# Optimization experiments

Measured on AMD Instinct MI355X. Metric: run time of the kernel, lower is better.

Reference implementation:

```python
import jax, jax.numpy as jnp
import numpy as np

B, LQ, E = 32, 64, 512
NF, FL, D = 10, 40, 512
H, A, R, V = 512, 512, 1024, 50257
NEG = -1e9


def setup_inputs() -> dict:
    key = jax.random.key(0)
    ks = jax.random.split(key, 20)
    s = 0.02
    return {
        'bq': jax.random.normal(ks[0], (B, LQ, E), jnp.float32),
        'fe': jax.random.normal(ks[1], (B, NF, FL, D), jnp.float32),
        'h0': jax.random.normal(ks[2], (B, H), jnp.float32),
        'c0': jax.random.normal(ks[3], (B, H), jnp.float32),
        'prev_emb': jax.random.normal(ks[4], (B, E), jnp.float32),
        'Wq_enc': jax.random.normal(ks[5], (E, A), jnp.float32) * s,
        'Wq_dec': jax.random.normal(ks[6], (H, A), jnp.float32) * s,
        'vq': jax.random.normal(ks[7], (A,), jnp.float32) * s,
        'Wf_enc': jax.random.normal(ks[8], (D, A), jnp.float32) * s,
        'Wf_dec': jax.random.normal(ks[9], (H, A), jnp.float32) * s,
        'vf': jax.random.normal(ks[10], (A,), jnp.float32) * s,
        'lstm_kernel': jax.random.normal(ks[11], (E + D + E, 4 * H), jnp.float32) * s,
        'lstm_rec': jax.random.normal(ks[12], (H, 4 * H), jnp.float32) * s,
        'lstm_bias': jnp.zeros((4 * H,), jnp.float32),
        'Wr': jax.random.normal(ks[13], (H, R), jnp.float32) * s,
        'br': jnp.zeros((R,), jnp.float32),
        'Ur': jax.random.normal(ks[14], (E + D + E, R), jnp.float32) * s,
        'bu': jnp.zeros((R,), jnp.float32),
        'Vr': jax.random.normal(ks[15], (E, R), jnp.float32) * s,
        'bv': jnp.zeros((R,), jnp.float32),
        'Wy': jax.random.normal(ks[16], (R // 2, V), jnp.float32) * s,
        'by': jnp.zeros((V,), jnp.float32),
        'q_mask': jnp.ones((B, LQ), bool),
        'f_mask': jnp.ones((B, NF, FL), bool),
    }


def reference(bq, fe, h0, c0, prev_emb, Wq_enc, Wq_dec, vq, Wf_enc, Wf_dec, vf,
              lstm_kernel, lstm_rec, lstm_bias, Wr, br, Ur, bu, Vr, bv, Wy, by,
              q_mask, f_mask):
    # --- question additive attention: softmax over seq axis ---
    q_scores = jnp.tanh(jnp.einsum('ble,ea->bla', bq, Wq_enc)
                        + (h0 @ Wq_dec)[:, None, :]) @ vq          # [B, Lq]
    q_logits = jnp.where(q_mask, q_scores, NEG)
    q_w = jax.nn.softmax(q_logits, axis=1)
    q_vec = jnp.einsum('bl,ble->be', q_w, bq)                      # [B, E]

    # --- facts attention: score all positions, keep top fact_len, renormalize ---
    f_scores = jnp.tanh(jnp.einsum('bnld,da->bnla', fe, Wf_enc)
                        + (h0 @ Wf_dec)[:, None, None, :]) @ vf    # [B, nf, fl]
    f_logits = jnp.where(f_mask, f_scores, NEG).reshape(fe.shape[0], -1)  # [B, nf*fl]
    fe_flat = fe.reshape(fe.shape[0], -1, fe.shape[-1])            # [B, nf*fl, D]
    top_scores, top_idx = jax.lax.top_k(f_logits, fe.shape[2])     # k = fact_len
    top_w = jax.nn.softmax(top_scores, axis=-1)                    # [B, fl]
    sel = jnp.take_along_axis(fe_flat, top_idx[:, :, None], axis=1)  # [B, fl, D]
    f_vec = jnp.einsum('bk,bkd->bd', top_w, sel)                   # [B, D]

    # --- LSTM cell (keras gate order i, f, g, o) ---
    x = jnp.concatenate([prev_emb, f_vec, q_vec], axis=1)          # [B, 2E+D]
    z = x @ lstm_kernel + h0 @ lstm_rec + lstm_bias
    i, f, g, o = jnp.split(z, 4, axis=-1)
    c = jax.nn.sigmoid(f) * c0 + jax.nn.sigmoid(i) * jnp.tanh(g)
    h = jax.nn.sigmoid(o) * jnp.tanh(c)

    # --- readout: three-branch dense + maxout + vocab projection ---
    r = (h @ Wr + br) + (x @ Ur + bu) + (q_vec @ Vr + bv)          # [B, R]
    m = r.reshape(r.shape[0], R // 2, 2).max(axis=-1)              # maxout -> [B, R/2]
    logits = m @ Wy + by                                           # [B, V]
    return logits, h, c, q_vec, q_logits
```

## Files before the change

kernel.cpp:

```cpp
#include <hip/hip_runtime.h>
#include <hip/hip_bf16.h>

#define B_ 32
#define LQ_ 64
#define E_ 512
#define NFL_ 400
#define D_ 512
#define H_ 512
#define A_ 512
#define R_ 1024
#define V_ 50257
#define X_ 1536
#define FL_ 40

#define O_H  1608224L
#define O_C  1624608L
#define O_QV 1640992L
#define O_QL 1657376L

typedef __bf16 bf16;
typedef __bf16 bf16x2 __attribute__((ext_vector_type(2)));
typedef __bf16 bf16x8 __attribute__((ext_vector_type(8)));
typedef float f32x4 __attribute__((ext_vector_type(4)));

__device__ inline float fexp(float x) { return __expf(x); }
__device__ inline float ftanh(float x) { return 1.0f - 2.0f / (fexp(2.0f * x) + 1.0f); }
__device__ inline float fsigm(float x) { return 1.0f / (1.0f + fexp(-x)); }

__global__ void k_transpose(const float* __restrict__ W0, const float* __restrict__ W1,
                            bf16* __restrict__ T0, bf16* __restrict__ T1) {
    __shared__ float tile[32][33];
    const float* src = blockIdx.z ? W1 : W0;
    bf16* dst = blockIdx.z ? T1 : T0;
    int k0 = blockIdx.y * 32, n0 = blockIdx.x * 32;
    int tx = threadIdx.x, ty = threadIdx.y;
    tile[ty][tx] = src[(k0 + ty) * 512 + n0 + tx];
    __syncthreads();
    dst[(n0 + ty) * 512 + k0 + tx] = (bf16)tile[tx][ty];
}

__global__ void k_proj(const float* __restrict__ h0, const float* __restrict__ Wq_dec,
                       const float* __restrict__ Wf_dec, float* __restrict__ dq,
                       float* __restrict__ df) {
    int b = blockIdx.y;
    int n = blockIdx.x * 256 + threadIdx.x;
    __shared__ float hl[H_];
    hl[threadIdx.x] = h0[b * H_ + threadIdx.x];
    hl[threadIdx.x + 256] = h0[b * H_ + threadIdx.x + 256];
    __syncthreads();
    const float* W = (n < A_) ? Wq_dec : Wf_dec;
    int col = n & 511;
    float acc = 0.f;
    #pragma unroll 8
    for (int k = 0; k < H_; ++k) acc += hl[k] * W[k * A_ + col];
    float* o = (n < A_) ? dq : df;
    o[b * A_ + col] = acc;
}

__global__ void k_copyprev(const float* __restrict__ pe, float* __restrict__ xb) {
    int idx = blockIdx.x * 256 + threadIdx.x;
    int b = idx >> 9, e = idx & 511;
    xb[b * X_ + e] = pe[idx];
}

__launch_bounds__(256)
__global__ void k_attn(const float* __restrict__ Amat, const bf16* __restrict__ Bt,
                       const float* __restrict__ proj, const float* __restrict__ vvec,
                       float* __restrict__ outv, int rows_per_b) {
    __shared__ bf16 al[32][520];
    int tid = threadIdx.x;
    int row0 = blockIdx.x * 32;
    #pragma unroll 8
    for (int it = 0; it < 32; ++it) {
        int i2 = it * 256 + tid;
        int r = i2 >> 8, c2 = i2 & 255;
        float2 f = *(const float2*)(Amat + (long)(row0 + r) * 512 + c2 * 2);
        bf16x2 t; t[0] = (bf16)f.x; t[1] = (bf16)f.y;
        *(bf16x2*)&al[r][c2 * 2] = t;
    }
    __syncthreads();
    int wid = tid >> 6, lane = tid & 63, q = lane >> 4, ln = lane & 15;
    int nbase = wid * 128;
    f32x4 acc[2][8];
    #pragma unroll
    for (int i = 0; i < 2; ++i)
        #pragma unroll
        for (int f = 0; f < 8; ++f) acc[i][f] = (f32x4){0.f, 0.f, 0.f, 0.f};
    for (int kk = 0; kk < 16; ++kk) {
        bf16x8 a0 = *(const bf16x8*)&al[ln][kk * 32 + q * 8];
        bf16x8 a1 = *(const bf16x8*)&al[16 + ln][kk * 32 + q * 8];
        #pragma unroll
        for (int f = 0; f < 8; ++f) {
            bf16x8 bb = *(const bf16x8*)(Bt + (long)(nbase + f * 16 + ln) * 512 + kk * 32 + q * 8);
            acc[0][f] = __builtin_amdgcn_mfma_f32_16x16x32_bf16(a0, bb, acc[0][f], 0, 0, 0);
            acc[1][f] = __builtin_amdgcn_mfma_f32_16x16x32_bf16(a1, bb, acc[1][f], 0, 0, 0);
        }
    }
    #pragma unroll
    for (int h2 = 0; h2 < 2; ++h2) {
        #pragma unroll
        for (int r = 0; r < 4; ++r) {
            int row = row0 + h2 * 16 + q * 4 + r;
            const float* pv = proj + (row / rows_per_b) * A_;
            float s = 0.f;
            #pragma unroll
            for (int f = 0; f < 8; ++f) {
                int n = nbase + f * 16 + ln;
                s += ftanh(acc[h2][f][r] + pv[n]) * vvec[n];
            }
            s += __shfl_xor(s, 1, 64); s += __shfl_xor(s, 2, 64);
            s += __shfl_xor(s, 4, 64); s += __shfl_xor(s, 8, 64);
            if (ln == 0) atomicAdd(outv + row, s);
        }
    }
}

__global__ void k_qsoft(const float* __restrict__ qsc, const float* __restrict__ bq,
                        float* __restrict__ out, float* __restrict__ xb) {
    int b = blockIdx.x, tid = threadIdx.x;
    __shared__ float w[LQ_];
    if (tid < 64) {
        float s = qsc[b * 64 + tid];
        out[O_QL + b * 64 + tid] = s;
        float m = s;
        for (int o = 32; o >= 1; o >>= 1) m = fmaxf(m, __shfl_xor(m, o, 64));
        float e = fexp(s - m);
        float sum = e;
        for (int o = 32; o >= 1; o >>= 1) sum += __shfl_xor(sum, o, 64);
        w[tid] = e / sum;
    }
    __syncthreads();
    #pragma unroll
    for (int e0 = 0; e0 < 2; ++e0) {
        int e = e0 * 256 + tid;
        float acc = 0.f;
        for (int l = 0; l < 64; ++l) acc += w[l] * bq[(b * 64 + l) * E_ + e];
        out[O_QV + b * E_ + e] = acc;
        xb[b * X_ + 1024 + e] = acc;
    }
}

__global__ void k_ftopk(const float* __restrict__ fl, const float* __restrict__ fe,
                        float* __restrict__ xb) {
    int b = blockIdx.x, tid = threadIdx.x;
    __shared__ float selw[FL_];
    __shared__ int   seli[FL_];
    if (tid < 64) {
        int lane = tid;
        float mv[7];
        #pragma unroll
        for (int s = 0; s < 7; ++s) {
            int idx = lane + s * 64;
            mv[s] = (idx < NFL_) ? fl[b * NFL_ + idx] : -1e30f;
        }
        float myv = -1e30f; int myi = 0; float v0 = 0.f;
        for (int j = 0; j < FL_; ++j) {
            float bv = -1e30f; int bi = 1 << 30;
            #pragma unroll
            for (int s = 0; s < 7; ++s) {
                int idx = lane + s * 64;
                if (mv[s] > bv || (mv[s] == bv && idx < bi)) { bv = mv[s]; bi = idx; }
            }
            for (int o = 1; o < 64; o <<= 1) {
                float ov = __shfl_xor(bv, o, 64); int oi = __shfl_xor(bi, o, 64);
                if (ov > bv || (ov == bv && oi < bi)) { bv = ov; bi = oi; }
            }
            if ((bi & 63) == lane) mv[bi >> 6] = -1e30f;
            if (lane == j) { myv = bv; myi = bi; }
            if (j == 0) v0 = bv;
        }
        float e = (lane < FL_) ? fexp(myv - v0) : 0.f;
        float sum = e;
        for (int o = 32; o >= 1; o >>= 1) sum += __shfl_xor(sum, o, 64);
        if (lane < FL_) { selw[lane] = e / sum; seli[lane] = myi; }
    }
    __syncthreads();
    #pragma unroll
    for (int d0 = 0; d0 < 2; ++d0) {
        int d = d0 * 256 + tid;
        float acc = 0.f;
        for (int j = 0; j < FL_; ++j) acc += selw[j] * fe[(long)(b * NFL_ + seli[j]) * D_ + d];
        xb[b * X_ + 512 + d] = acc;
    }
}

__launch_bounds__(256)
__global__ void k_gemm32(const float* __restrict__ Am, int lda,
                         const float* __restrict__ Bm, int N,
                         int kchunk, float* __restrict__ Cacc) {
    extern __shared__ bf16 alds[];
    int S = kchunk + 8;
    int tid = threadIdx.x;
    int k0 = blockIdx.y * kchunk;
    for (int i2 = tid; i2 < 16 * kchunk; i2 += 256) {
        int e2 = i2 * 2;
        int m = e2 / kchunk;
        int k = e2 - m * kchunk;
        float2 f = *(const float2*)(Am + (long)m * lda + k0 + k);
        bf16x2 t; t[0] = (bf16)f.x; t[1] = (bf16)f.y;
        *(bf16x2*)&alds[m * S + k] = t;
    }
    __syncthreads();
    int wid = tid >> 6, lane = tid & 63, q = lane >> 4, ln = lane & 15;
    int n = blockIdx.x * 64 + wid * 16 + ln;
    f32x4 acc0 = {0.f, 0.f, 0.f, 0.f}, acc1 = {0.f, 0.f, 0.f, 0.f};
    int steps = kchunk >> 5;
    for (int kk = 0; kk < steps; ++kk) {
        bf16x8 a0 = *(const bf16x8*)&alds[ln * S + kk * 32 + q * 8];
        bf16x8 a1 = *(const bf16x8*)&alds[(16 + ln) * S + kk * 32 + q * 8];
        bf16x8 bb;
        int kg = k0 + kk * 32 + q * 8;
        #pragma unroll
        for (int j = 0; j < 8; ++j) bb[j] = (bf16)Bm[(long)(kg + j) * N + n];
        acc0 = __builtin_amdgcn_mfma_f32_16x16x32_bf16(a0, bb, acc0, 0, 0, 0);
        acc1 = __builtin_amdgcn_mfma_f32_16x16x32_bf16(a1, bb, acc1, 0, 0, 0);
    }
    #pragma unroll
    for (int r = 0; r < 4; ++r) {
        atomicAdd(Cacc + (q * 4 + r) * N + n, acc0[r]);
        atomicAdd(Cacc + (16 + q * 4 + r) * N + n, acc1[r]);
    }
}

__global__ void k_gates(const float* __restrict__ z, const float* __restrict__ lb,
                        const float* __restrict__ c0, float* __restrict__ out,
                        float* __restrict__ hb) {
    int idx = blockIdx.x * 256 + threadIdx.x;
    int b = idx >> 9, hh = idx & 511;
    const float* zb = z + b * 2048;
    float iv = zb[hh]        + lb[hh];
    float fv = zb[512 + hh]  + lb[512 + hh];
    float gv = zb[1024 + hh] + lb[1024 + hh];
    float ov = zb[1536 + hh] + lb[1536 + hh];
    float c = fsigm(fv) * c0[idx] + fsigm(iv) * ftanh(gv);
    float h = fsigm(ov) * ftanh(c);
    out[O_H + idx] = h;
    out[O_C + idx] = c;
    hb[idx] = h;
}

__global__ void k_maxout(const float* __restrict__ r, const float* __restrict__ br,
                         const float* __restrict__ bu, const float* __restrict__ bv,
                         bf16* __restrict__ mb) {
    int idx = blockIdx.x * 256 + threadIdx.x;
    int b = idx >> 9, j = idx & 511;
    int n0 = 2 * j, n1 = 2 * j + 1;
    float r0 = r[b * R_ + n0] + br[n0] + bu[n0] + bv[n0];
    float r1 = r[b * R_ + n1] + br[n1] + bu[n1] + bv[n1];
    mb[idx] = (bf16)fmaxf(r0, r1);
}

__launch_bounds__(256)
__global__ void k_vocab(const bf16* __restrict__ mtab, const float* __restrict__ Wy,
                        const float* __restrict__ by, float* __restrict__ out) {
    __shared__ bf16 al[32][520];
    int tid = threadIdx.x;
    #pragma unroll
    for (int it = 0; it < 8; ++it) {
        int e = it * 2048 + tid * 8;
        int b = e >> 9, k = e & 511;
        *(bf16x8*)&al[b][k] = *(const bf16x8*)(mtab + e);
    }
    __syncthreads();
    int wid = tid >> 6, lane = tid & 63, q = lane >> 4, ln = lane & 15;
    int c = blockIdx.x * 64 + wid * 16 + ln;
    int cc = (c < V_) ? c : (V_ - 1);
    const float* wp = Wy + cc;
    f32x4 acc0 = {0.f, 0.f, 0.f, 0.f}, acc1 = {0.f, 0.f, 0.f, 0.f};
    float bnf[8];
    #pragma unroll
    for (int j = 0; j < 8; ++j) bnf[j] = wp[(long)(q * 8 + j) * V_];
    #pragma unroll 1
    for (int kk = 0; kk < 16; ++kk) {
        float bcur[8];
        #pragma unroll
        for (int j = 0; j < 8; ++j) bcur[j] = bnf[j];
        if (kk < 15) {
            #pragma unroll
            for (int j = 0; j < 8; ++j)
                bnf[j] = wp[(long)((kk + 1) * 32 + q * 8 + j) * V_];
        }
        bf16x8 bb;
        #pragma unroll
        for (int j = 0; j < 8; ++j) bb[j] = (bf16)bcur[j];
        bf16x8 a0 = *(const bf16x8*)&al[ln][kk * 32 + q * 8];
        bf16x8 a1 = *(const bf16x8*)&al[16 + ln][kk * 32 + q * 8];
        acc0 = __builtin_amdgcn_mfma_f32_16x16x32_bf16(a0, bb, acc0, 0, 0, 0);
        acc1 = __builtin_amdgcn_mfma_f32_16x16x32_bf16(a1, bb, acc1, 0, 0, 0);
    }
    if (c < V_) {
        float bias = by[c];
        #pragma unroll
        for (int r = 0; r < 4; ++r) {
            out[(long)(q * 4 + r) * V_ + c]      = acc0[r] + bias;
            out[(long)(16 + q * 4 + r) * V_ + c] = acc1[r] + bias;
        }
    }
}

extern "C" void kernel_launch(void* const* d_in, const int* in_sizes, int n_in,
                              void* d_out, int out_size, void* d_ws, size_t ws_size,
                              hipStream_t stream) {
    const float* bq     = (const float*)d_in[0];
    const float* fe     = (const float*)d_in[1];
    const float* h0     = (const float*)d_in[2];
    const float* c0     = (const float*)d_in[3];
    const float* prev   = (const float*)d_in[4];
    const float* Wq_enc = (const float*)d_in[5];
    const float* Wq_dec = (const float*)d_in[6];
    const float* vq     = (const float*)d_in[7];
    const float* Wf_enc = (const float*)d_in[8];
    const float* Wf_dec = (const float*)d_in[9];
    const float* vf     = (const float*)d_in[10];
    const float* lk     = (const float*)d_in[11];
    const float* lr     = (const float*)d_in[12];
    const float* lb     = (const float*)d_in[13];
    const float* Wr     = (const float*)d_in[14];
    const float* br     = (const float*)d_in[15];
    const float* Ur     = (const float*)d_in[16];
    const float* bu     = (const float*)d_in[17];
    const float* Vr     = (const float*)d_in[18];
    const float* bv     = (const float*)d_in[19];
    const float* Wy     = (const float*)d_in[20];
    const float* by     = (const float*)d_in[21];

    char* sc = (char*)d_out;
    bf16*  Wq_t = (bf16*)(sc + 0);
    bf16*  Wf_t = (bf16*)(sc + 524288);
    float* dq   = (float*)(sc + 1048576);
    float* df   = (float*)(sc + 1114112);
    float* zrec = (float*)(sc + 1179648);
    float* qsc  = (float*)(sc + 1441792);
    float* flog = (float*)(sc + 1449984);
    float* rws  = (float*)(sc + 1501184);
    float* xb   = (float*)(sc + 1632256);
    float* hb   = (float*)(sc + 1828864);
    bf16*  mb   = (bf16*)d_ws;

    float* out = (float*)d_out;

    hipMemsetAsync(zrec, 0, 452608, stream);

    k_transpose<<<dim3(16, 16, 2), dim3(32, 32), 0, stream>>>(Wq_enc, Wf_enc, Wq_t, Wf_t);
    k_proj<<<dim3(4, 32), 256, 0, stream>>>(h0, Wq_dec, Wf_dec, dq, df);
    k_copyprev<<<64, 256, 0, stream>>>(prev, xb);
    k_attn<<<64, 256, 0, stream>>>(bq, Wq_t, dq, vq, qsc, LQ_);
    k_attn<<<400, 256, 0, stream>>>(fe, Wf_t, df, vf, flog, NFL_);
    k_qsoft<<<32, 256, 0, stream>>>(qsc, bq, out, xb);
    k_ftopk<<<32, 256, 0, stream>>>(flog, fe, xb);
    k_gemm32<<<dim3(32, 4), 256, 32 * (384 + 8) * 2, stream>>>(xb, X_, lk, 2048, 384, zrec);
    k_gemm32<<<dim3(32, 2), 256, 32 * (256 + 8) * 2, stream>>>(h0, 512, lr, 2048, 256, zrec);
    k_gates<<<64, 256, 0, stream>>>(zrec, lb, c0, out, hb);
    k_gemm32<<<dim3(16, 2), 256, 32 * (256 + 8) * 2, stream>>>(hb, 512, Wr, 1024, 256, rws);
    k_gemm32<<<dim3(16, 4), 256, 32 * (384 + 8) * 2, stream>>>(xb, X_, Ur, 1024, 384, rws);
    k_gemm32<<<dim3(16, 2), 256, 32 * (256 + 8) * 2, stream>>>(xb + 1024, X_, Vr, 1024, 256, rws);
    k_maxout<<<64, 256, 0, stream>>>(rws, br, bu, bv, mb);
    k_vocab<<<786, 256, 0, stream>>>(mb, Wy, by, out);
}
```

Measured before the change: 471.7 us.

## Merge independent kernel launches into combined multi-role kernels

Merges transpose, decoder projection and prev-embedding copy into one launch. It also merges the two attention launches, the question-softmax and fact top-k kernels, and four independent GEMMs (LSTM input/recurrent plus the Ur/Vr readout branches) into single grids dispatched by block index. The aim is to cut launch overhead and the serialization between small, independent kernels. The Ur/Vr GEMMs now run before the gates kernel, and some blocks in the merged GEMM grid exit early, leaving idle blocks.

Measured after the change: 388.6 us. 1.21x faster.

```diff
diff --git a/kernel.cpp b/kernel.cpp
--- a/kernel.cpp
+++ b/kernel.cpp
@@ -27,49 +27,71 @@
 __device__ inline float ftanh(float x) { return 1.0f - 2.0f / (fexp(2.0f * x) + 1.0f); }
 __device__ inline float fsigm(float x) { return 1.0f / (1.0f + fexp(-x)); }
 
-__global__ void k_transpose(const float* __restrict__ W0, const float* __restrict__ W1,
-                            bf16* __restrict__ T0, bf16* __restrict__ T1) {
-    __shared__ float tile[32][33];
-    const float* src = blockIdx.z ? W1 : W0;
-    bf16* dst = blockIdx.z ? T1 : T0;
-    int k0 = blockIdx.y * 32, n0 = blockIdx.x * 32;
-    int tx = threadIdx.x, ty = threadIdx.y;
-    tile[ty][tx] = src[(k0 + ty) * 512 + n0 + tx];
-    __syncthreads();
-    dst[(n0 + ty) * 512 + k0 + tx] = (bf16)tile[tx][ty];
-}
-
-__global__ void k_proj(const float* __restrict__ h0, const float* __restrict__ Wq_dec,
-                       const float* __restrict__ Wf_dec, float* __restrict__ dq,
-                       float* __restrict__ df) {
-    int b = blockIdx.y;
-    int n = blockIdx.x * 256 + threadIdx.x;
-    __shared__ float hl[H_];
-    hl[threadIdx.x] = h0[b * H_ + threadIdx.x];
-    hl[threadIdx.x + 256] = h0[b * H_ + threadIdx.x + 256];
-    __syncthreads();
-    const float* W = (n < A_) ? Wq_dec : Wf_dec;
-    int col = n & 511;
-    float acc = 0.f;
-    #pragma unroll 8
-    for (int k = 0; k < H_; ++k) acc += hl[k] * W[k * A_ + col];
-    float* o = (n < A_) ? dq : df;
-    o[b * A_ + col] = acc;
-}
-
-__global__ void k_copyprev(const float* __restrict__ pe, float* __restrict__ xb) {
-    int idx = blockIdx.x * 256 + threadIdx.x;
-    int b = idx >> 9, e = idx & 511;
-    xb[b * X_ + e] = pe[idx];
-}
-
-__launch_bounds__(256)
-__global__ void k_attn(const float* __restrict__ Amat, const bf16* __restrict__ Bt,
-                       const float* __restrict__ proj, const float* __restrict__ vvec,
-                       float* __restrict__ outv, int rows_per_b) {
+__launch_bounds__(256)
+__global__ void k_pre(const float* __restrict__ W0, const float* __restrict__ W1,
+                      bf16* __restrict__ T0, bf16* __restrict__ T1,
+                      const float* __restrict__ h0, const float* __restrict__ Wq_dec,
+                      const float* __restrict__ Wf_dec, float* __restrict__ dq,
+                      float* __restrict__ df, const float* __restrict__ pe,
+                      float* __restrict__ xb) {
+    int bx = blockIdx.x;
+    if (bx < 512) {
+        __shared__ float tile[32][33];
+        int mat = bx >> 8, rest = bx & 255;
+        const float* src = mat ? W1 : W0;
+        bf16* dst = mat ? T1 : T0;
+        int k0 = (rest >> 4) * 32, n0 = (rest & 15) * 32;
+        int tx = threadIdx.x & 31, ty0 = threadIdx.x >> 5;
+        #pragma unroll
+        for (int r = 0; r < 4; ++r) {
+            int ty = ty0 + 8 * r;
+            tile[ty][tx] = src[(k0 + ty) * 512 + n0 + tx];
+        }
+        __syncthreads();
+        #pragma unroll
+        for (int r = 0; r < 4; ++r) {
+            int ty = ty0 + 8 * r;
+            dst[(n0 + ty) * 512 + k0 + tx] = (bf16)tile[tx][ty];
+        }
+    } else if (bx < 640) {
+        __shared__ float hl[H_];
+        int pb = bx - 512;
+        int b = pb >> 2;
+        int n = (pb & 3) * 256 + threadIdx.x;
+        hl[threadIdx.x] = h0[b * H_ + threadIdx.x];
+        hl[threadIdx.x + 256] = h0[b * H_ + threadIdx.x + 256];
+        __syncthreads();
+        const float* W = (n < A_) ? Wq_dec : Wf_dec;
+        int col = n & 511;
+        float acc = 0.f;
+        #pragma unroll 8
+        for (int k = 0; k < H_; ++k) acc += hl[k] * W[k * A_ + col];
+        ((n < A_) ? dq : df)[b * A_ + col] = acc;
+    } else {
+        int idx = (bx - 640) * 256 + threadIdx.x;
+        int b = idx >> 9, e = idx & 511;
+        xb[b * X_ + e] = pe[idx];
+    }
+}
+
+__launch_bounds__(256)
+__global__ void k_attn2(const float* __restrict__ bq, const float* __restrict__ fe,
+                        const bf16* __restrict__ Btq, const bf16* __restrict__ Btf,
+                        const float* __restrict__ dq, const float* __restrict__ df,
+                        const float* __restrict__ vq, const float* __restrict__ vf,
+                        float* __restrict__ qsc, float* __restrict__ flog) {
+    bool isq = blockIdx.x < 64;
+    const float* Amat = isq ? bq : fe;
+    const bf16* Bt = isq ? Btq : Btf;
+    const float* proj = isq ? dq : df;
+    const float* vvec = isq ? vq : vf;
+    float* outv = isq ? qsc : flog;
+    int rows_per_b = isq ? LQ_ : NFL_;
+    int bx = isq ? blockIdx.x : blockIdx.x - 64;
+
     __shared__ bf16 al[32][520];
     int tid = threadIdx.x;
-    int row0 = blockIdx.x * 32;
+    int row0 = bx * 32;
     #pragma unroll 8
     for (int it = 0; it < 32; ++it) {
         int i2 = it * 256 + tid;
@@ -115,83 +137,83 @@
     }
 }
 
-__global__ void k_qsoft(const float* __restrict__ qsc, const float* __restrict__ bq,
-                        float* __restrict__ out, float* __restrict__ xb) {
-    int b = blockIdx.x, tid = threadIdx.x;
-    __shared__ float w[LQ_];
-    if (tid < 64) {
-        float s = qsc[b * 64 + tid];
-        out[O_QL + b * 64 + tid] = s;
-        float m = s;
-        for (int o = 32; o >= 1; o >>= 1) m = fmaxf(m, __shfl_xor(m, o, 64));
-        float e = fexp(s - m);
-        float sum = e;
-        for (int o = 32; o >= 1; o >>= 1) sum += __shfl_xor(sum, o, 64);
-        w[tid] = e / sum;
-    }
-    __syncthreads();
-    #pragma unroll
-    for (int e0 = 0; e0 < 2; ++e0) {
-        int e = e0 * 256 + tid;
-        float acc = 0.f;
-        for (int l = 0; l < 64; ++l) acc += w[l] * bq[(b * 64 + l) * E_ + e];
-        out[O_QV + b * E_ + e] = acc;
-        xb[b * X_ + 1024 + e] = acc;
-    }
-}
-
-__global__ void k_ftopk(const float* __restrict__ fl, const float* __restrict__ fe,
-                        float* __restrict__ xb) {
-    int b = blockIdx.x, tid = threadIdx.x;
-    __shared__ float selw[FL_];
-    __shared__ int   seli[FL_];
-    if (tid < 64) {
-        int lane = tid;
-        float mv[7];
-        #pragma unroll
-        for (int s = 0; s < 7; ++s) {
-            int idx = lane + s * 64;
-            mv[s] = (idx < NFL_) ? fl[b * NFL_ + idx] : -1e30f;
-        }
-        float myv = -1e30f; int myi = 0; float v0 = 0.f;
-        for (int j = 0; j < FL_; ++j) {
-            float bv = -1e30f; int bi = 1 << 30;
+__launch_bounds__(256)
+__global__ void k_soft(const float* __restrict__ qsc, const float* __restrict__ bq,
+                       float* __restrict__ out, float* __restrict__ xb,
+                       const float* __restrict__ fl, const float* __restrict__ fe) {
+    int tid = threadIdx.x;
+    if (blockIdx.x < 32) {
+        int b = blockIdx.x;
+        __shared__ float w[LQ_];
+        if (tid < 64) {
+            float s = qsc[b * 64 + tid];
+            out[O_QL + b * 64 + tid] = s;
+            float m = s;
+            for (int o = 32; o >= 1; o >>= 1) m = fmaxf(m, __shfl_xor(m, o, 64));
+            float e = fexp(s - m);
+            float sum = e;
+            for (int o = 32; o >= 1; o >>= 1) sum += __shfl_xor(sum, o, 64);
+            w[tid] = e / sum;
+        }
+        __syncthreads();
+        #pragma unroll
+        for (int e0 = 0; e0 < 2; ++e0) {
+            int e = e0 * 256 + tid;
+            float acc = 0.f;
+            for (int l = 0; l < 64; ++l) acc += w[l] * bq[(b * 64 + l) * E_ + e];
+            out[O_QV + b * E_ + e] = acc;
+            xb[b * X_ + 1024 + e] = acc;
+        }
+    } else {
+        int b = blockIdx.x - 32;
+        __shared__ float selw[FL_];
+        __shared__ int   seli[FL_];
+        if (tid < 64) {
+            int lane = tid;
+            float mv[7];
             #pragma unroll
             for (int s = 0; s < 7; ++s) {
                 int idx = lane + s * 64;
-                if (mv[s] > bv || (mv[s] == bv && idx < bi)) { bv = mv[s]; bi = idx; }
+                mv[s] = (idx < NFL_) ? fl[b * NFL_ + idx] : -1e30f;
             }
-            for (int o = 1; o < 64; o <<= 1) {
-                float ov = __shfl_xor(bv, o, 64); int oi = __shfl_xor(bi, o, 64);
-                if (ov > bv || (ov == bv && oi < bi)) { bv = ov; bi = oi; }
+            float myv = -1e30f; int myi = 0; float v0 = 0.f;
+            for (int j = 0; j < FL_; ++j) {
+                float bv = -1e30f; int bi = 1 << 30;
+                #pragma unroll
+                for (int s = 0; s < 7; ++s) {
+                    int idx = lane + s * 64;
+                    if (mv[s] > bv || (mv[s] == bv && idx < bi)) { bv = mv[s]; bi = idx; }
+                }
+                for (int o = 1; o < 64; o <<= 1) {
+                    float ov = __shfl_xor(bv, o, 64); int oi = __shfl_xor(bi, o, 64);
+                    if (ov > bv || (ov == bv && oi < bi)) { bv = ov; bi = oi; }
+                }
+                if ((bi & 63) == lane) mv[bi >> 6] = -1e30f;
+                if (lane == j) { myv = bv; myi = bi; }
+                if (j == 0) v0 = bv;
             }
-            if ((bi & 63) == lane) mv[bi >> 6] = -1e30f;
-            if (lane == j) { myv = bv; myi = bi; }
-            if (j == 0) v0 = bv;
-        }
-        float e = (lane < FL_) ? fexp(myv - v0) : 0.f;
-        float sum = e;
-        for (int o = 32; o >= 1; o >>= 1) sum += __shfl_xor(sum, o, 64);
-        if (lane < FL_) { selw[lane] = e / sum; seli[lane] = myi; }
-    }
-    __syncthreads();
-    #pragma unroll
-    for (int d0 = 0; d0 < 2; ++d0) {
-        int d = d0 * 256 + tid;
-        float acc = 0.f;
-        for (int j = 0; j < FL_; ++j) acc += selw[j] * fe[(long)(b * NFL_ + seli[j]) * D_ + d];
-        xb[b * X_ + 512 + d] = acc;
-    }
-}
-
-__launch_bounds__(256)
-__global__ void k_gemm32(const float* __restrict__ Am, int lda,
-                         const float* __restrict__ Bm, int N,
-                         int kchunk, float* __restrict__ Cacc) {
-    extern __shared__ bf16 alds[];
+            float e = (lane < FL_) ? fexp(myv - v0) : 0.f;
+            float sum = e;
+            for (int o = 32; o >= 1; o >>= 1) sum += __shfl_xor(sum, o, 64);
+            if (lane < FL_) { selw[lane] = e / sum; seli[lane] = myi; }
+        }
+        __syncthreads();
+        #pragma unroll
+        for (int d0 = 0; d0 < 2; ++d0) {
+            int d = d0 * 256 + tid;
+            float acc = 0.f;
+            for (int j = 0; j < FL_; ++j) acc += selw[j] * fe[(long)(b * NFL_ + seli[j]) * D_ + d];
+            xb[b * X_ + 512 + d] = acc;
+        }
+    }
+}
+
+__device__ __forceinline__ void gemm32_body(
+        bf16* alds, const float* __restrict__ Am, int lda,
+        const float* __restrict__ Bm, int N, int kchunk, int k0,
+        float* __restrict__ Cacc, int gx) {
     int S = kchunk + 8;
     int tid = threadIdx.x;
-    int k0 = blockIdx.y * kchunk;
     for (int i2 = tid; i2 < 16 * kchunk; i2 += 256) {
         int e2 = i2 * 2;
         int m = e2 / kchunk;
@@ -202,7 +224,7 @@
     }
     __syncthreads();
     int wid = tid >> 6, lane = tid & 63, q = lane >> 4, ln = lane & 15;
-    int n = blockIdx.x * 64 + wid * 16 + ln;
+    int n = gx * 64 + wid * 16 + ln;
     f32x4 acc0 = {0.f, 0.f, 0.f, 0.f}, acc1 = {0.f, 0.f, 0.f, 0.f};
     int steps = kchunk >> 5;
     for (int kk = 0; kk < steps; ++kk) {
@@ -220,6 +242,31 @@
         atomicAdd(Cacc + (q * 4 + r) * N + n, acc0[r]);
         atomicAdd(Cacc + (16 + q * 4 + r) * N + n, acc1[r]);
     }
+}
+
+__launch_bounds__(256)
+__global__ void k_gemmA(const float* __restrict__ xb, const float* __restrict__ h0,
+                        const float* __restrict__ lk, const float* __restrict__ lr,
+                        const float* __restrict__ Ur, const float* __restrict__ Vr,
+                        float* __restrict__ zrec, float* __restrict__ rws) {
+    __shared__ bf16 alds[32 * 392];
+    int y = blockIdx.y;
+    const float* Am; const float* Bm; float* Cacc;
+    int lda, kchunk, k0, N;
+    if (y < 4)       { Am = xb;        lda = X_;  kchunk = 384; k0 = y * 384;        Bm = lk; N = 2048; Cacc = zrec; }
+    else if (y < 6)  { Am = h0;        lda = 512; kchunk = 256; k0 = (y - 4) * 256;  Bm = lr; N = 2048; Cacc = zrec; }
+    else if (y < 10) { Am = xb;        lda = X_;  kchunk = 384; k0 = (y - 6) * 384;  Bm = Ur; N = 1024; Cacc = rws; }
+    else             { Am = xb + 1024; lda = X_;  kchunk = 256; k0 = (y - 10) * 256; Bm = Vr; N = 1024; Cacc = rws; }
+    if ((int)blockIdx.x * 64 >= N) return;
+    gemm32_body(alds, Am, lda, Bm, N, kchunk, k0, Cacc, blockIdx.x);
+}
+
+__launch_bounds__(256)
+__global__ void k_gemm32(const float* __restrict__ Am, int lda,
+                         const float* __restrict__ Bm, int N,
+                         int kchunk, float* __restrict__ Cacc) {
+    extern __shared__ bf16 alds[];
+    gemm32_body(alds, Am, lda, Bm, N, kchunk, blockIdx.y * kchunk, Cacc, blockIdx.x);
 }
 
 __global__ void k_gates(const float* __restrict__ z, const float* __restrict__ lb,
@@ -341,19 +388,13 @@
 
     hipMemsetAsync(zrec, 0, 452608, stream);
 
-    k_transpose<<<dim3(16, 16, 2), dim3(32, 32), 0, stream>>>(Wq_enc, Wf_enc, Wq_t, Wf_t);
-    k_proj<<<dim3(4, 32), 256, 0, stream>>>(h0, Wq_dec, Wf_dec, dq, df);
-    k_copyprev<<<64, 256, 0, stream>>>(prev, xb);
-    k_attn<<<64, 256, 0, stream>>>(bq, Wq_t, dq, vq, qsc, LQ_);
-    k_attn<<<400, 256, 0, stream>>>(fe, Wf_t, df, vf, flog, NFL_);
-    k_qsoft<<<32, 256, 0, stream>>>(qsc, bq, out, xb);
-    k_ftopk<<<32, 256, 0, stream>>>(flog, fe, xb);
-    k_gemm32<<<dim3(32, 4), 256, 32 * (384 + 8) * 2, stream>>>(xb, X_, lk, 2048, 384, zrec);
-    k_gemm32<<<dim3(32, 2), 256, 32 * (256 + 8) * 2, stream>>>(h0, 512, lr, 2048, 256, zrec);
+    k_pre<<<704, 256, 0, stream>>>(Wq_enc, Wf_enc, Wq_t, Wf_t, h0, Wq_dec, Wf_dec,
+                                   dq, df, prev, xb);
+    k_attn2<<<464, 256, 0, stream>>>(bq, fe, Wq_t, Wf_t, dq, df, vq, vf, qsc, flog);
+    k_soft<<<64, 256, 0, stream>>>(qsc, bq, out, xb, flog, fe);
+    k_gemmA<<<dim3(32, 12), 256, 0, stream>>>(xb, h0, lk, lr, Ur, Vr, zrec, rws);
     k_gates<<<64, 256, 0, stream>>>(zrec, lb, c0, out, hb);
     k_gemm32<<<dim3(16, 2), 256, 32 * (256 + 8) * 2, stream>>>(hb, 512, Wr, 1024, 256, rws);
-    k_gemm32<<<dim3(16, 4), 256, 32 * (384 + 8) * 2, stream>>>(xb, X_, Ur, 1024, 384, rws);
-    k_gemm32<<<dim3(16, 2), 256, 32 * (256 + 8) * 2, stream>>>(xb + 1024, X_, Vr, 1024, 256, rws);
     k_maxout<<<64, 256, 0, stream>>>(rws, br, bu, bv, mb);
     k_vocab<<<786, 256, 0, stream>>>(mb, Wy, by, out);
 }
```
